# Optimization experiments

Hardware: AMD Instinct MI355X
Metric: run time of the kernel (lower is better)

Reference implementation:

```python
import jax, jax.numpy as jnp
import numpy as np
from jax import lax

ORDER = 6
SAMPLES = 64
TOPK = 512
STRIDE = 2          # contour features are stride-2 w.r.t. input ('1' level)
NMS_THRESH = 0.2
REF_ITERS = 4
REF_MARGIN = 3.0
HC = WC = 256       # contour-feature grid
HF = WF = 512       # full-res (refinement) grid


def conv2d(x, w, b=None, pad=0):
    # x: [B,C,H,W], w: [O,I,kh,kw]
    y = lax.conv_general_dilated(x, w, (1, 1), [(pad, pad), (pad, pad)],
                                 dimension_numbers=("NCHW", "OIHW", "NCHW"))
    if b is not None:
        y = y + b[None, :, None, None]
    return y


def setup_inputs() -> dict:
    key = jax.random.key(0)
    ks = jax.random.split(key, 16)
    s = 0.05
    d = {
        "contour_features": jax.random.normal(ks[0], (4, 64, HC, WC), jnp.float32),
        "enc_score_features": jax.random.normal(ks[1], (4, 64, HC, WC), jnp.float32),
        "refinement_features": jax.random.normal(ks[2], (4, 32, HF, WF), jnp.float32),
        "enc_refinement_features": jax.random.normal(ks[3], (4, 32, HF, WF), jnp.float32),
        # learned params
        "w_score_reduce": jax.random.normal(ks[4], (64, 128, 1, 1)) * s,
        "w_score": jax.random.normal(ks[5], (2, 64, 7, 7)) * s,
        "b_score": jnp.zeros((2,), jnp.float32),
        "w_loc": jax.random.normal(ks[6], (2, 64, 7, 7)) * s,
        "b_loc": jnp.zeros((2,), jnp.float32),
        "w_fourier": jax.random.normal(ks[7], (ORDER * 4, 64, 7, 7)) * s,
        "b_fourier": jnp.zeros((ORDER * 4,), jnp.float32),
        "w_ref_reduce": jax.random.normal(ks[8], (32, 64, 1, 1)) * s,
        "w_ref": jax.random.normal(ks[9], (2, 32, 7, 7)) * s,
        "b_ref": jnp.zeros((2,), jnp.float32),
    }
    return d


def _pairwise_iou(boxes):
    # boxes: [K,4] as (x1,y1,x2,y2)
    x1, y1, x2, y2 = boxes[:, 0], boxes[:, 1], boxes[:, 2], boxes[:, 3]
    area = jnp.maximum(x2 - x1, 0.) * jnp.maximum(y2 - y1, 0.)
    ix1 = jnp.maximum(x1[:, None], x1[None, :])
    iy1 = jnp.maximum(y1[:, None], y1[None, :])
    ix2 = jnp.minimum(x2[:, None], x2[None, :])
    iy2 = jnp.minimum(y2[:, None], y2[None, :])
    inter = jnp.maximum(ix2 - ix1, 0.) * jnp.maximum(iy2 - iy1, 0.)
    union = area[:, None] + area[None, :] - inter
    return inter / jnp.maximum(union, 1e-8)


def _nms_keep(boxes, valid):
    # boxes sorted by descending score. Sequential greedy NMS.
    iou = _pairwise_iou(boxes)  # [K,K]
    idx = jnp.arange(TOPK)

    def body(i, keep):
        sup = (iou[i] > NMS_THRESH) & keep[i] & (idx > i)
        return keep & ~sup

    keep = lax.fori_loop(0, TOPK, body, valid)
    return keep


def _forward(contour_features, enc_score_features, refinement_features,
             enc_refinement_features, w_score_reduce, w_score, b_score,
             w_loc, b_loc, w_fourier, b_fourier, w_ref_reduce, w_ref, b_ref):
    B = contour_features.shape[0]
    # ---- dense heads (CPNCore.forward) ----
    sf = conv2d(jnp.concatenate([contour_features, enc_score_features], 1), w_score_reduce)
    score_logits = conv2d(sf, w_score, b_score, pad=3)            # [B,2,HC,WC]
    log_scores = jax.nn.log_softmax(score_logits, axis=1)
    locations = conv2d(contour_features, w_loc, b_loc, pad=3)     # [B,2,HC,WC]
    fourier = conv2d(contour_features, w_fourier, b_fourier, pad=3)  # [B,4*ORDER,HC,WC]

    rf = conv2d(jnp.concatenate([refinement_features, enc_refinement_features], 1), w_ref_reduce)
    refinement = jnp.tanh(conv2d(rf, w_ref, b_ref, pad=3)) * REF_MARGIN  # [B,2,HF,WF]

    # ---- proposal selection: top-K foreground scores ----
    fg = jnp.exp(log_scores[:, 1])                                # [B,HC,WC]
    fg_flat = fg.reshape(B, -1)
    top_scores, top_idx = lax.top_k(fg_flat, TOPK)                # [B,K] sorted desc
    valid = top_scores > 0.5                                      # score_thresh

    gy = (top_idx // WC).astype(jnp.float32)
    gx = (top_idx % WC).astype(jnp.float32)

    def gather_ch(t):  # t: [B,C,HC,WC] -> [B,K,C]
        C = t.shape[1]
        tf = t.reshape(B, C, -1)
        out = jnp.take_along_axis(tf, top_idx[:, None, :].repeat(C, axis=1), axis=2)
        return out.transpose(0, 2, 1)

    loc = gather_ch(locations)                                    # [B,K,2] (x,y offsets)
    fr = gather_ch(fourier).reshape(B, TOPK, ORDER, 4)            # a_x,b_x,a_y,b_y

    cx = (gx + loc[..., 0]) * STRIDE
    cy = (gy + loc[..., 1]) * STRIDE

    # ---- fourier -> contour sampling ----
    t = jnp.arange(SAMPLES, dtype=jnp.float32) / SAMPLES
    k = jnp.arange(1, ORDER + 1, dtype=jnp.float32)
    ang = 2.0 * jnp.pi * k[:, None] * t[None, :]                  # [ORDER,SAMPLES]
    cos, sin = jnp.cos(ang), jnp.sin(ang)
    px = jnp.einsum('bko,os->bks', fr[..., 0], cos) + jnp.einsum('bko,os->bks', fr[..., 1], sin)
    py = jnp.einsum('bko,os->bks', fr[..., 2], cos) + jnp.einsum('bko,os->bks', fr[..., 3], sin)
    contour = jnp.stack([px * STRIDE + cx[..., None], py * STRIDE + cy[..., None]], -1)  # [B,K,S,2]

    # ---- iterative local refinement (nearest-neighbor gather) ----
    ref_flat = refinement.reshape(B, 2, -1)
    for _ in range(REF_ITERS):
        xi = jnp.clip(jnp.round(contour[..., 0]), 0, WF - 1).astype(jnp.int32)
        yi = jnp.clip(jnp.round(contour[..., 1]), 0, HF - 1).astype(jnp.int32)
        flat = (yi * WF + xi).reshape(B, 1, -1)                   # [B,1,K*S]
        off = jnp.take_along_axis(ref_flat, flat.repeat(2, axis=1), axis=2)
        off = off.reshape(B, 2, TOPK, SAMPLES).transpose(0, 2, 3, 1)  # [B,K,S,2]
        contour = contour + off

    # ---- boxes + NMS ----
    boxes = jnp.concatenate([contour.min(axis=2), contour.max(axis=2)], -1)  # [B,K,4]
    keep = jax.vmap(_nms_keep)(boxes, valid)
    return contour, top_scores, keep, boxes


def reference(contour_features, enc_score_features, refinement_features,
              enc_refinement_features, w_score_reduce, w_score, b_score,
              w_loc, b_loc, w_fourier, b_fourier, w_ref_reduce, w_ref, b_ref):
    return _forward(contour_features, enc_score_features, refinement_features,
                    enc_refinement_features, w_score_reduce, w_score, b_score,
                    w_loc, b_loc, w_fourier, b_fourier, w_ref_reduce, w_ref, b_ref)
```

## Files before the change

kernel.cpp:

```cpp
#include <hip/hip_runtime.h>
#include <math.h>

#define WS_D     0ull
#define WS_REF   1048576ull
#define WS_SPART 9437184ull
#define WS_WSE   13631488ull
#define WS_WRE   13731840ull
#define WS_WG    13782016ull
#define WS_TIDX  14108160ull
#define WS_GATH  14116352ull
#define WS_TRIG  14329344ull
#define WS_CLIST 14332416ull
#define WS_CNT   14365184ull
#define WS_PAIRS 14365200ull
#define WS_WRE32 14430736ull
#define WS_WSE32 14455824ull
#define WS_END   14506000ull

__global__ __launch_bounds__(256) void cpn_prep_kernel(
    const float* __restrict__ w_score_reduce, const float* __restrict__ w_score,
    const float* __restrict__ w_loc, const float* __restrict__ w_fourier,
    const float* __restrict__ w_ref_reduce, const float* __restrict__ w_ref,
    double* __restrict__ wse, double* __restrict__ wre, float* __restrict__ wg,
    float* __restrict__ trig, float* __restrict__ wre32, float* __restrict__ wse32)
{
    int i = blockIdx.x * 256 + threadIdx.x;
    if (i < 12544) {
        int o = i / 6272;
        int rem = i % 6272;
        int c = rem / 49, r = rem % 49;
        double a = 0.0;
        for (int m = 0; m < 64; ++m)
            a += (double)w_score[(o*64 + m)*49 + r] * (double)w_score_reduce[m*128 + c];
        wse[i] = a;
    } else if (i < 12544 + 6272) {
        int t = i - 12544;
        int o = t / 3136;
        int rem = t % 3136;
        int c = rem / 49, r = rem % 49;
        double a = 0.0;
        for (int m = 0; m < 32; ++m)
            a += (double)w_ref[(o*32 + m)*49 + r] * (double)w_ref_reduce[m*64 + c];
        wre[t] = a;
    } else if (i < 12544 + 6272 + 81536) {
        int t = i - 18816;
        int tap = t / 26, o = t % 26;
        wg[t] = (o < 2) ? w_loc[o*3136 + tap] : w_fourier[(o - 2)*3136 + tap];
    } else if (i < 100352 + 768) {
        int t = i - 100352;
        int cs = t / 384;
        int k = (t % 384) / 64, s = t % 64;
        const float TWO_PI_F = (float)6.283185307179586;
        float a1 = TWO_PI_F * (float)(k + 1);
        float tf = (float)s * 0.015625f;
        float ang = a1 * tf;
        double av = (double)ang;
        trig[t] = (cs == 0) ? (float)cos(av) : (float)sin(av);
    } else if (i < 101120 + 6272) {
        int t = i - 101120;
        int c = t / 98, r98 = t % 98;
        int ky = r98 / 14, q = r98 % 14;
        int kx = q >> 1, o = q & 1;
        int rr = ky*7 + kx;
        double a = 0.0;
        for (int m = 0; m < 32; ++m)
            a += (double)w_ref[(o*32 + m)*49 + rr] * (double)w_ref_reduce[m*64 + c];
        wre32[t] = (float)a;
    } else if (i < 107392 + 12544) {
        int t = i - 107392;
        int c = t / 98, r98 = t % 98;
        int ky = r98 / 14, q = r98 % 14;
        int kx = q >> 1, o = q & 1;
        int rr = ky*7 + kx;
        double a = 0.0;
        for (int m = 0; m < 64; ++m)
            a += (double)w_score[(o*64 + m)*49 + rr] * (double)w_score_reduce[m*128 + c];
        wse32[t] = (float)a;
    }
}

__global__ __launch_bounds__(512) void cpn_score_dense_kernel(
    const float* __restrict__ cf, const float* __restrict__ esf,
    const float* __restrict__ wse32, float2* __restrict__ partial)
{
    __shared__ __align__(16) float spatch[2][1672];
    const int tid  = threadIdx.x;
    const int t2   = tid & 255;
    const int h    = tid >> 8;
    const int b    = blockIdx.z >> 1;
    const int srch = blockIdx.z & 1;
    const float* src = srch ? esf : cf;
    const float* sbase = src + ((size_t)(b*64 + h*32) << 16);
    const int row0 = blockIdx.y * 32;
    const int col0 = blockIdx.x * 32;
    const int ty   = t2 >> 3;
    const int txg  = t2 & 7;
    const int cbase = srch*64 + h*32;

    float acc0[4] = {0.f,0.f,0.f,0.f};
    float acc1[4] = {0.f,0.f,0.f,0.f};
    float sreg[6];

    {
        #pragma unroll
        for (int k = 0; k < 6; ++k) {
            int i = k*256 + t2; float v = 0.f;
            if (i < 1520) {
                int r = i/40, j = i%40;
                int gy = row0 - 3 + r, gx = col0 - 4 + j;
                if ((unsigned)gy < 256u && (unsigned)gx < 256u) v = sbase[gy*256 + gx];
            }
            sreg[k] = v;
        }
    }

    for (int c = 0; c < 32; ++c) {
        #pragma unroll
        for (int k = 0; k < 6; ++k) {
            int i = k*256 + t2;
            if (i < 1520) spatch[h][(i/40)*44 + (i%40)] = sreg[k];
        }
        __syncthreads();
        if (c + 1 < 32) {
            const float* sp = sbase + ((size_t)(c+1) << 16);
            #pragma unroll
            for (int k = 0; k < 6; ++k) {
                int i = k*256 + t2; float v = 0.f;
                if (i < 1520) {
                    int r = i/40, j = i%40;
                    int gy = row0 - 3 + r, gx = col0 - 4 + j;
                    if ((unsigned)gy < 256u && (unsigned)gx < 256u) v = sp[gy*256 + gx];
                }
                sreg[k] = v;
            }
        }
        int cg = __builtin_amdgcn_readfirstlane(cbase + c);
        const float* wc = wse32 + cg*98;
        #pragma unroll
        for (int ky = 0; ky < 7; ++ky) {
            const float4* pr4 = reinterpret_cast<const float4*>(&spatch[h][(ty+ky)*44 + txg*4]);
            float4 A = pr4[0], B2 = pr4[1], C2 = pr4[2];
            float rv[12] = {A.x,A.y,A.z,A.w,B2.x,B2.y,B2.z,B2.w,C2.x,C2.y,C2.z,C2.w};
            const float* wp = wc + ky*14;
            float wv[14];
            #pragma unroll
            for (int q = 0; q < 14; ++q) wv[q] = wp[q];
            #pragma unroll
            for (int kx = 0; kx < 7; ++kx) {
                float w0 = wv[2*kx], w1 = wv[2*kx+1];
                #pragma unroll
                for (int p = 0; p < 4; ++p) {
                    float v = rv[p + kx + 1];
                    acc0[p] = fmaf(w0, v, acc0[p]);
                    acc1[p] = fmaf(w1, v, acc1[p]);
                }
            }
        }
        __syncthreads();
    }

    float* cmb = &spatch[0][0];
    if (h == 1) {
        #pragma unroll
        for (int p = 0; p < 4; ++p) { cmb[t2*8 + p] = acc0[p]; cmb[t2*8 + 4 + p] = acc1[p]; }
    }
    __syncthreads();
    if (h == 0) {
        int y = row0 + ty;
        #pragma unroll
        for (int p = 0; p < 4; ++p) {
            float s0 = acc0[p] + cmb[t2*8 + p];
            float s1 = acc1[p] + cmb[t2*8 + 4 + p];
            int x = col0 + txg*4 + p;
            float2 v; v.x = s0; v.y = s1;
            partial[(size_t)(srch*4 + b)*65536 + y*256 + x] = v;
        }
    }
}

__global__ __launch_bounds__(256) void cpn_dcomb_kernel(
    const float2* __restrict__ partial, float* __restrict__ d)
{
    int i = blockIdx.x * 256 + threadIdx.x;
    int b = i >> 16, px = i & 65535;
    float2 p0 = partial[(size_t)b*65536 + px];
    float2 p1 = partial[(size_t)(4 + b)*65536 + px];
    float l0 = p0.x + p1.x;
    float l1 = p0.y + p1.y;
    d[i] = l1 - l0;
}

__global__ __launch_bounds__(512) void cpn_ref_conv_kernel(
    const float* __restrict__ rff, const float* __restrict__ erf,
    const float* __restrict__ wre32, const float* __restrict__ b_ref,
    float* __restrict__ refmap)
{
    __shared__ __align__(16) float4 patches[2][38][19];
    const int tid = threadIdx.x;
    const int t2  = tid & 255;
    const int h   = tid >> 8;
    const int b   = blockIdx.z;
    const int row0 = blockIdx.y * 32;
    const int col0 = blockIdx.x * 64;
    const int tyg = t2 & 31;
    const int txg = t2 >> 5;
    const float* sbase = (h ? erf : rff) + ((size_t)(b*32) << 18);

    int   st_r[3], st_f[3];
    long  st_off[3];
    bool  st_ok[3];
    #pragma unroll
    for (int k = 0; k < 3; ++k) {
        int i = k*256 + t2;
        int r = i / 18, f = i % 18;
        int gy = row0 - 3 + r, gx = col0 - 4 + 4*f;
        st_r[k] = r; st_f[k] = f;
        st_ok[k] = (i < 684) && ((unsigned)gy < 512u) && ((unsigned)gx < 509u);
        st_off[k] = (long)gy * 512 + gx;
    }

    float4 s4[3];
    {
        #pragma unroll
        for (int k = 0; k < 3; ++k) {
            float4 v = {0.f,0.f,0.f,0.f};
            if (st_ok[k]) v = *reinterpret_cast<const float4*>(sbase + st_off[k]);
            s4[k] = v;
        }
    }

    float acc0[8] = {0,0,0,0,0,0,0,0};
    float acc1[8] = {0,0,0,0,0,0,0,0};

    for (int c = 0; c < 32; ++c) {
        #pragma unroll
        for (int k = 0; k < 3; ++k) {
            int i = k*256 + t2;
            if (i < 684) patches[h][st_r[k]][st_f[k]] = s4[k];
        }
        __syncthreads();
        if (c + 1 < 32) {
            const float* sp = sbase + ((size_t)(c+1) << 18);
            #pragma unroll
            for (int k = 0; k < 3; ++k) {
                float4 v = {0.f,0.f,0.f,0.f};
                if (st_ok[k]) v = *reinterpret_cast<const float4*>(sp + st_off[k]);
                s4[k] = v;
            }
        }
        int cg = __builtin_amdgcn_readfirstlane(h*32 + c);
        const float* wc = wre32 + cg*98;
        #pragma unroll
        for (int pr = 0; pr < 7; ++pr) {
            int row = tyg + pr;
            float4 A  = patches[h][row][2*txg + 0];
            float4 B2 = patches[h][row][2*txg + 1];
            float4 C2 = patches[h][row][2*txg + 2];
            float4 D2 = patches[h][row][2*txg + 3];
            float rv[16] = {A.x,A.y,A.z,A.w,B2.x,B2.y,B2.z,B2.w,
                            C2.x,C2.y,C2.z,C2.w,D2.x,D2.y,D2.z,D2.w};
            const float* wp = wc + pr*14;
            float wv[14];
            #pragma unroll
            for (int q = 0; q < 14; ++q) wv[q] = wp[q];
            #pragma unroll
            for (int kx = 0; kx < 7; ++kx) {
                float w0 = wv[2*kx], w1 = wv[2*kx+1];
                #pragma unroll
                for (int p = 0; p < 8; ++p) {
                    float v = rv[p + kx + 1];
                    acc0[p] = fmaf(w0, v, acc0[p]);
                    acc1[p] = fmaf(w1, v, acc1[p]);
                }
            }
        }
        __syncthreads();
    }

    float* cmb = reinterpret_cast<float*>(&patches[0][0][0]);
    if (h == 1) {
        #pragma unroll
        for (int p = 0; p < 8; ++p) { cmb[t2*16 + p] = acc0[p]; cmb[t2*16 + 8 + p] = acc1[p]; }
    }
    __syncthreads();
    if (h == 0) {
        float br0 = b_ref[0], br1 = b_ref[1];
        int y = row0 + tyg;
        int x0 = col0 + txg*8;
        #pragma unroll
        for (int p = 0; p < 8; ++p) {
            float s0 = acc0[p] + cmb[t2*16 + p];
            float s1 = acc1[p] + cmb[t2*16 + 8 + p];
            refmap[((size_t)(b*2 + 0)*512 + y)*512 + x0 + p] = tanhf(s0 + br0) * 3.0f;
            refmap[((size_t)(b*2 + 1)*512 + y)*512 + x0 + p] = tanhf(s1 + br1) * 3.0f;
        }
    }
}

__device__ __forceinline__ void cpn_find_bucket(
    unsigned int* hist, unsigned int* seg, int nb, int target, int tid,
    int* s_bsel, int* s_cnt)
{
    int nseg = nb / 32;
    for (int t = tid; t < nseg; t += 1024) {
        unsigned int s = 0;
        for (int q = 0; q < 32; ++q) s += hist[t*32 + q];
        seg[t] = s;
    }
    __syncthreads();
    if (tid == 0) {
        int cum = 0, sg = 0;
        for (int jj = nseg - 1; jj >= 0; --jj) {
            int c = (int)seg[jj];
            if (cum + c >= target) { sg = jj; break; }
            cum += c;
        }
        int bs = sg*32;
        for (int jj = sg*32 + 31; jj >= sg*32; --jj) {
            int c = (int)hist[jj];
            if (cum + c >= target) { bs = jj; break; }
            cum += c;
        }
        *s_bsel = bs; *s_cnt = cum;
    }
    __syncthreads();
}

__device__ __forceinline__ unsigned int cpn_fkey(float v) {
    unsigned int u = __float_as_uint(v);
    return (u & 0x80000000u) ? ~u : (u | 0x80000000u);
}

__global__ __launch_bounds__(1024) void cpn_select_kernel(
    const float* __restrict__ d, int* __restrict__ clist, int* __restrict__ cnt)
{
    const int b = blockIdx.x;
    const int tid = threadIdx.x;
    const float* f = d + (size_t)b * 65536;

    __shared__ unsigned int hist[2048];
    __shared__ unsigned int seg[64];
    __shared__ int s_b, s_c, s_n;

    const int bitsA[3]  = {11,11,10};
    const int shiftA[3] = {21,10,0};

    unsigned int prefix = 0;
    int target = 512;
    for (int pass = 0; pass < 3; ++pass) {
        int sh = shiftA[pass], nb = 1 << bitsA[pass];
        for (int i = tid; i < 2048; i += 1024) hist[i] = 0;
        __syncthreads();
        if (pass == 0) {
            for (int i = tid; i < 65536; i += 1024) {
                unsigned int k = cpn_fkey(f[i]);
                atomicAdd(&hist[k >> 21], 1u);
            }
        } else {
            int hs = sh + bitsA[pass];
            for (int i = tid; i < 65536; i += 1024) {
                unsigned int k = cpn_fkey(f[i]);
                if ((k >> hs) == prefix)
                    atomicAdd(&hist[(k >> sh) & (nb-1)], 1u);
            }
        }
        __syncthreads();
        cpn_find_bucket(hist, seg, nb, target, tid, &s_b, &s_c);
        prefix = (prefix << bitsA[pass]) | (unsigned)s_b;
        target -= s_c;
    }
    float T = (prefix & 0x80000000u) ? __uint_as_float(prefix & 0x7FFFFFFFu)
                                     : __uint_as_float(~prefix);
    float tval = T - 0.0625f;

    if (tid == 0) s_n = 0;
    __syncthreads();
    for (int i = tid; i < 65536; i += 1024) {
        if (f[i] >= tval) {
            int q = atomicAdd(&s_n, 1);
            if (q < 2048) clist[b*2048 + q] = i;
        }
    }
    __syncthreads();
    if (tid == 0) cnt[b] = (s_n > 2048) ? 2048 : s_n;
}

__global__ __launch_bounds__(256) void cpn_recompute_kernel(
    const float* __restrict__ cf, const float* __restrict__ esf,
    const double* __restrict__ wse, const float* __restrict__ b_score,
    const int* __restrict__ clist, const int* __restrict__ cnt,
    uint2* __restrict__ pairs)
{
    const int b = blockIdx.y, q = blockIdx.x, tid = threadIdx.x;
    const int n = cnt[b];
    if (q >= n) {
        if (tid == 0) { uint2 pd; pd.x = 0u; pd.y = 0x7FFFFFFFu; pairs[b*2048 + q] = pd; }
        return;
    }
    const int idx = clist[b*2048 + q];
    const int gy = idx >> 8, gx = idx & 255;

    double L0 = 0.0, L1 = 0.0;
    for (int t = tid; t < 6272; t += 256) {
        int c = t / 49, r = t % 49, ky = r / 7, kx = r % 7;
        int y = gy + ky - 3, x = gx + kx - 3;
        float v = 0.f;
        if ((unsigned)y < 256u && (unsigned)x < 256u) {
            const float* src = (c < 64) ? cf : esf;
            v = src[((size_t)(b*64 + (c & 63)) << 16) + y*256 + x];
        }
        double dv = (double)v;
        L0 = fma(dv, wse[c*49 + r], L0);
        L1 = fma(dv, wse[6272 + c*49 + r], L1);
    }
    #pragma unroll
    for (int off = 32; off; off >>= 1) {
        L0 += __shfl_down(L0, off, 64);
        L1 += __shfl_down(L1, off, 64);
    }
    __shared__ double red[4][2];
    int w = tid >> 6, lane = tid & 63;
    if (lane == 0) { red[w][0] = L0; red[w][1] = L1; }
    __syncthreads();
    if (tid == 0) {
        double S0 = red[0][0] + red[1][0] + red[2][0] + red[3][0];
        double S1 = red[0][1] + red[1][1] + red[2][1] + red[3][1];
        float l0f = (float)(S0 + (double)b_score[0]);
        float l1f = (float)(S1 + (double)b_score[1]);
        float m  = fmaxf(l0f, l1f);
        float e0 = (float)exp((double)(l0f - m));
        float e1 = (float)exp((double)(l1f - m));
        float s  = e0 + e1;
        float lg = (float)log((double)s);
        float ls1 = (l1f - m) - lg;
        float fgv = (float)exp((double)ls1);
        uint2 pr; pr.x = __float_as_uint(fgv); pr.y = (unsigned)idx;
        pairs[b*2048 + q] = pr;
    }
}

__global__ __launch_bounds__(1024) void cpn_sortk_kernel(
    const uint2* __restrict__ pairs, int* __restrict__ tidx,
    float* __restrict__ tscores)
{
    const int b = blockIdx.x;
    const int tid = threadIdx.x;
    __shared__ unsigned int key[2048];
    __shared__ int sidx[2048];

    for (int q = tid; q < 2048; q += 1024) {
        uint2 pr = pairs[b*2048 + q];
        key[q] = pr.x; sidx[q] = (int)pr.y;
    }
    __syncthreads();
    for (int kk = 2; kk <= 2048; kk <<= 1)
        for (int jj = kk >> 1; jj > 0; jj >>= 1) {
            for (int i = tid; i < 2048; i += 1024) {
                int ixj = i ^ jj;
                if (ixj > i) {
                    unsigned int ka = key[i], kc = key[ixj];
                    int ia = sidx[i], ic = sidx[ixj];
                    bool up = ((i & kk) == 0);
                    bool aBefore = (ka > kc) || (ka == kc && ia < ic);
                    if (up ? !aBefore : aBefore) {
                        key[i] = kc; key[ixj] = ka;
                        sidx[i] = ic; sidx[ixj] = ia;
                    }
                }
            }
            __syncthreads();
        }
    for (int q = tid; q < 512; q += 1024) {
        tscores[b*512 + q] = __uint_as_float(key[q]);
        tidx[b*512 + q] = sidx[q];
    }
}

__global__ __launch_bounds__(256) void cpn_gather_conv_kernel(
    const float* __restrict__ cf, const float* __restrict__ wg,
    const float* __restrict__ b_loc, const float* __restrict__ b_fourier,
    const int* __restrict__ tidx, float* __restrict__ gath)
{
    const int b = blockIdx.y, p = blockIdx.x, tid = threadIdx.x;
    const int idx = tidx[b*512 + p];
    const int gy = idx >> 8, gx = idx & 255;

    double part[26];
    #pragma unroll
    for (int o = 0; o < 26; ++o) part[o] = 0.0;

    for (int t = tid; t < 3136; t += 256) {
        int c = t / 49, rr = t % 49, ky = rr / 7, kx = rr % 7;
        int y = gy + ky - 3, x = gx + kx - 3;
        float v = 0.f;
        if ((unsigned)y < 256u && (unsigned)x < 256u)
            v = cf[((size_t)(b*64 + c)*256 + y)*256 + x];
        const float* wr = wg + t*26;
        double dv = (double)v;
        #pragma unroll
        for (int o = 0; o < 26; ++o) part[o] = fma(dv, (double)wr[o], part[o]);
    }
    #pragma unroll
    for (int o = 0; o < 26; ++o)
        for (int off = 32; off; off >>= 1) part[o] += __shfl_down(part[o], off, 64);

    __shared__ double red[4][26];
    int w = tid >> 6, lane = tid & 63;
    if (lane == 0) {
        #pragma unroll
        for (int o = 0; o < 26; ++o) red[w][o] = part[o];
    }
    __syncthreads();
    if (tid < 26) {
        double s = red[0][tid] + red[1][tid] + red[2][tid] + red[3][tid];
        s += (tid < 2) ? (double)b_loc[tid] : (double)b_fourier[tid - 2];
        gath[((size_t)b*512 + p)*26 + tid] = (float)s;
    }
}

__global__ __launch_bounds__(64) void cpn_contour_kernel(
    const float* __restrict__ gath, const int* __restrict__ tidx,
    const float* __restrict__ refmap, const float* __restrict__ trig,
    float* __restrict__ out_contour, float* __restrict__ out_boxes)
{
    const int bp = blockIdx.x;
    const int b = bp >> 9;
    const int s = threadIdx.x;
    const float* g = gath + (size_t)bp * 26;
    const int idx = tidx[bp];
    const int gy = idx >> 8, gx = idx & 255;

    float cx = ((float)gx + g[0]) * 2.0f;
    float cy = ((float)gy + g[1]) * 2.0f;

    float sxc = 0.f, sxs = 0.f, syc = 0.f, sys = 0.f;
    #pragma unroll
    for (int k = 0; k < 6; ++k) {
        float cs = trig[k*64 + s];
        float sn = trig[384 + k*64 + s];
        float t0 = g[2 + k*4 + 0] * cs; asm volatile("" : "+v"(t0)); sxc += t0;
        float t1 = g[2 + k*4 + 1] * sn; asm volatile("" : "+v"(t1)); sxs += t1;
        float t2 = g[2 + k*4 + 2] * cs; asm volatile("" : "+v"(t2)); syc += t2;
        float t3 = g[2 + k*4 + 3] * sn; asm volatile("" : "+v"(t3)); sys += t3;
    }
    float px = sxc + sxs;
    float py = syc + sys;
    float x = px * 2.0f; asm volatile("" : "+v"(x)); x += cx;
    float y = py * 2.0f; asm volatile("" : "+v"(y)); y += cy;

    const float* r0 = refmap + (size_t)b * 2 * 262144;
    const float* r1 = r0 + 262144;
    #pragma unroll
    for (int it = 0; it < 4; ++it) {
        float xr = rintf(x); xr = fminf(fmaxf(xr, 0.f), 511.f);
        float yr = rintf(y); yr = fminf(fmaxf(yr, 0.f), 511.f);
        int xi = (int)xr, yi = (int)yr;
        x += r0[yi*512 + xi];
        y += r1[yi*512 + xi];
    }

    out_contour[((size_t)bp*64 + s)*2 + 0] = x;
    out_contour[((size_t)bp*64 + s)*2 + 1] = y;

    float mnx = x, mxx = x, mny = y, mxy = y;
    #pragma unroll
    for (int off = 32; off; off >>= 1) {
        mnx = fminf(mnx, __shfl_xor(mnx, off, 64));
        mny = fminf(mny, __shfl_xor(mny, off, 64));
        mxx = fmaxf(mxx, __shfl_xor(mxx, off, 64));
        mxy = fmaxf(mxy, __shfl_xor(mxy, off, 64));
    }
    if (s == 0) {
        out_boxes[bp*4 + 0] = mnx;
        out_boxes[bp*4 + 1] = mny;
        out_boxes[bp*4 + 2] = mxx;
        out_boxes[bp*4 + 3] = mxy;
    }
}

__global__ __launch_bounds__(512) void cpn_nms_kernel(
    const float* __restrict__ boxes, const float* __restrict__ scores,
    float* __restrict__ keep_out)
{
    const int b = blockIdx.x;
    const int j = threadIdx.x;
    __shared__ float X1[512], Y1[512], X2[512], Y2[512], AR[512];
    __shared__ int keep[512];

    const float* bb = boxes + b*512*4;
    float x1 = bb[j*4+0], y1 = bb[j*4+1], x2 = bb[j*4+2], y2 = bb[j*4+3];
    float aj = fmaxf(x2 - x1, 0.f) * fmaxf(y2 - y1, 0.f);
    X1[j] = x1; Y1[j] = y1; X2[j] = x2; Y2[j] = y2; AR[j] = aj;
    keep[j] = (scores[b*512 + j] > 0.5f) ? 1 : 0;
    __syncthreads();

    for (int i = 0; i < 512; ++i) {
        if (keep[i] && j > i) {
            float ix1 = fmaxf(x1, X1[i]);
            float iy1 = fmaxf(y1, Y1[i]);
            float ix2 = fminf(x2, X2[i]);
            float iy2 = fminf(y2, Y2[i]);
            float inter = fmaxf(ix2 - ix1, 0.f) * fmaxf(iy2 - iy1, 0.f);
            float uni = (aj + AR[i]) - inter;
            float iou = inter / fmaxf(uni, 1e-8f);
            if (iou > 0.2f) keep[j] = 0;
        }
        __syncthreads();
    }
    keep_out[b*512 + j] = keep[j] ? 1.0f : 0.0f;
}

extern "C" void kernel_launch(void* const* d_in, const int* in_sizes, int n_in,
                              void* d_out, int out_size, void* d_ws, size_t ws_size,
                              hipStream_t stream)
{
    if (ws_size < WS_END) return;

    const float* cf   = (const float*)d_in[0];
    const float* esf  = (const float*)d_in[1];
    const float* rff  = (const float*)d_in[2];
    const float* erf  = (const float*)d_in[3];
    const float* w_sr = (const float*)d_in[4];
    const float* w_s  = (const float*)d_in[5];
    const float* b_s  = (const float*)d_in[6];
    const float* w_l  = (const float*)d_in[7];
    const float* b_l  = (const float*)d_in[8];
    const float* w_f  = (const float*)d_in[9];
    const float* b_f  = (const float*)d_in[10];
    const float* w_rr = (const float*)d_in[11];
    const float* w_r  = (const float*)d_in[12];
    const float* b_r  = (const float*)d_in[13];

    char* ws = (char*)d_ws;
    float*  dbuf = (float*)(ws + WS_D);
    float*  refm = (float*)(ws + WS_REF);
    float2* spart = (float2*)(ws + WS_SPART);
    double* wse  = (double*)(ws + WS_WSE);
    double* wre  = (double*)(ws + WS_WRE);
    float*  wg   = (float*)(ws + WS_WG);
    int*    tidx = (int*)(ws + WS_TIDX);
    float*  gath = (float*)(ws + WS_GATH);
    float*  trig = (float*)(ws + WS_TRIG);
    int*    clist = (int*)(ws + WS_CLIST);
    int*    cnt  = (int*)(ws + WS_CNT);
    uint2*  pairs = (uint2*)(ws + WS_PAIRS);
    float*  wre32 = (float*)(ws + WS_WRE32);
    float*  wse32 = (float*)(ws + WS_WSE32);

    float* out_contour = (float*)d_out;
    float* out_scores  = out_contour + 262144;
    float* out_keep    = out_scores + 2048;
    float* out_boxes   = out_keep + 2048;

    cpn_prep_kernel<<<dim3(469), dim3(256), 0, stream>>>(
        w_sr, w_s, w_l, w_f, w_rr, w_r, wse, wre, wg, trig, wre32, wse32);
    cpn_score_dense_kernel<<<dim3(8, 8, 8), dim3(512), 0, stream>>>(
        cf, esf, wse32, spart);
    cpn_ref_conv_kernel<<<dim3(8, 16, 4), dim3(512), 0, stream>>>(
        rff, erf, wre32, b_r, refm);
    cpn_dcomb_kernel<<<dim3(1024), dim3(256), 0, stream>>>(spart, dbuf);
    cpn_select_kernel<<<dim3(4), dim3(1024), 0, stream>>>(dbuf, clist, cnt);
    cpn_recompute_kernel<<<dim3(2048, 4), dim3(256), 0, stream>>>(
        cf, esf, wse, b_s, clist, cnt, pairs);
    cpn_sortk_kernel<<<dim3(4), dim3(1024), 0, stream>>>(pairs, tidx, out_scores);
    cpn_gather_conv_kernel<<<dim3(512, 4), dim3(256), 0, stream>>>(
        cf, wg, b_l, b_f, tidx, gath);
    cpn_contour_kernel<<<dim3(2048), dim3(64), 0, stream>>>(
        gath, tidx, refm, trig, out_contour, out_boxes);
    cpn_nms_kernel<<<dim3(4), dim3(512), 0, stream>>>(
        out_boxes, out_scores, out_keep);
}
```

Measured before the change: 673.4 us.

## Stage conv input patches via direct global-to-LDS loads with double buffering

Both the dense score conv and the refinement conv now load input channel patches with global_load_lds straight into a double-buffered shared-memory patch, replacing the register staging and separate LDS store. This removes VGPR staging and the store step, and drops one barrier per channel iteration, so the next channel's load overlaps compute on the current buffer. Out-of-bounds slots are zeroed once at start and never rewritten. The score-conv patch also switches to float4 rows with 40-wide stride and 4-aligned loads. A risk is correctness of the async LDS writes, since there is no explicit vmcnt wait before the single barrier that precedes use.

```diff
diff --git a/kernel.cpp b/kernel.cpp
--- a/kernel.cpp
+++ b/kernel.cpp
@@ -16,6 +16,9 @@
 #define WS_WRE32 14430736ull
 #define WS_WSE32 14455824ull
 #define WS_END   14506000ull
+
+typedef __attribute__((address_space(1))) const void cpn_gv;
+typedef __attribute__((address_space(3))) void cpn_lv;
 
 __global__ __launch_bounds__(256) void cpn_prep_kernel(
     const float* __restrict__ w_score_reduce, const float* __restrict__ w_score,
@@ -83,10 +86,11 @@
     const float* __restrict__ cf, const float* __restrict__ esf,
     const float* __restrict__ wse32, float2* __restrict__ partial)
 {
-    __shared__ __align__(16) float spatch[2][1672];
+    __shared__ __align__(16) float4 patch[2][2][380];
     const int tid  = threadIdx.x;
     const int t2   = tid & 255;
     const int h    = tid >> 8;
+    const int wv   = t2 >> 6;
     const int b    = blockIdx.z >> 1;
     const int srch = blockIdx.z & 1;
     const float* src = srch ? esf : cf;
@@ -97,57 +101,59 @@
     const int txg  = t2 & 7;
     const int cbase = srch*64 + h*32;
 
+    long st_off[2];
+    bool st_ok[2];
+    #pragma unroll
+    for (int k = 0; k < 2; ++k) {
+        int i = k*256 + t2;
+        int r = i / 10, f = i % 10;
+        int gy = row0 - 3 + r, gx = col0 - 4 + 4*f;
+        st_ok[k] = (i < 380) && ((unsigned)gy < 256u) && ((unsigned)gx < 253u);
+        st_off[k] = (long)gy * 256 + gx;
+    }
+
+    float4 z4 = {0.f,0.f,0.f,0.f};
+    for (int i = tid; i < 2*2*380; i += 512) (&patch[0][0][0])[i] = z4;
+    __syncthreads();
+
+    #pragma unroll
+    for (int k = 0; k < 2; ++k)
+        if (st_ok[k])
+            __builtin_amdgcn_global_load_lds(
+                (cpn_gv*)(sbase + st_off[k]),
+                (cpn_lv*)&patch[h][0][k*256 + wv*64], 16, 0, 0);
+
     float acc0[4] = {0.f,0.f,0.f,0.f};
     float acc1[4] = {0.f,0.f,0.f,0.f};
-    float sreg[6];
-
-    {
-        #pragma unroll
-        for (int k = 0; k < 6; ++k) {
-            int i = k*256 + t2; float v = 0.f;
-            if (i < 1520) {
-                int r = i/40, j = i%40;
-                int gy = row0 - 3 + r, gx = col0 - 4 + j;
-                if ((unsigned)gy < 256u && (unsigned)gx < 256u) v = sbase[gy*256 + gx];
-            }
-            sreg[k] = v;
-        }
-    }
 
     for (int c = 0; c < 32; ++c) {
-        #pragma unroll
-        for (int k = 0; k < 6; ++k) {
-            int i = k*256 + t2;
-            if (i < 1520) spatch[h][(i/40)*44 + (i%40)] = sreg[k];
-        }
         __syncthreads();
         if (c + 1 < 32) {
             const float* sp = sbase + ((size_t)(c+1) << 16);
             #pragma unroll
-            for (int k = 0; k < 6; ++k) {
-                int i = k*256 + t2; float v = 0.f;
-                if (i < 1520) {
-                    int r = i/40, j = i%40;
-                    int gy = row0 - 3 + r, gx = col0 - 4 + j;
-                    if ((unsigned)gy < 256u && (unsigned)gx < 256u) v = sp[gy*256 + gx];
-                }
-                sreg[k] = v;
-            }
+            for (int k = 0; k < 2; ++k)
+                if (st_ok[k])
+                    __builtin_amdgcn_global_load_lds(
+                        (cpn_gv*)(sp + st_off[k]),
+                        (cpn_lv*)&patch[h][(c+1)&1][k*256 + wv*64], 16, 0, 0);
         }
         int cg = __builtin_amdgcn_readfirstlane(cbase + c);
         const float* wc = wse32 + cg*98;
+        const float4* pb = &patch[h][c & 1][0];
         #pragma unroll
         for (int ky = 0; ky < 7; ++ky) {
-            const float4* pr4 = reinterpret_cast<const float4*>(&spatch[h][(ty+ky)*44 + txg*4]);
-            float4 A = pr4[0], B2 = pr4[1], C2 = pr4[2];
+            int row = ty + ky;
+            float4 A  = pb[row*10 + txg + 0];
+            float4 B2 = pb[row*10 + txg + 1];
+            float4 C2 = pb[row*10 + txg + 2];
             float rv[12] = {A.x,A.y,A.z,A.w,B2.x,B2.y,B2.z,B2.w,C2.x,C2.y,C2.z,C2.w};
             const float* wp = wc + ky*14;
-            float wv[14];
+            float wv14[14];
             #pragma unroll
-            for (int q = 0; q < 14; ++q) wv[q] = wp[q];
+            for (int q = 0; q < 14; ++q) wv14[q] = wp[q];
             #pragma unroll
             for (int kx = 0; kx < 7; ++kx) {
-                float w0 = wv[2*kx], w1 = wv[2*kx+1];
+                float w0 = wv14[2*kx], w1 = wv14[2*kx+1];
                 #pragma unroll
                 for (int p = 0; p < 4; ++p) {
                     float v = rv[p + kx + 1];
@@ -156,10 +162,10 @@
                 }
             }
         }
-        __syncthreads();
-    }
-
-    float* cmb = &spatch[0][0];
+    }
+    __syncthreads();
+
+    float* cmb = reinterpret_cast<float*>(&patch[0][0][0]);
     if (h == 1) {
         #pragma unroll
         for (int p = 0; p < 4; ++p) { cmb[t2*8 + p] = acc0[p]; cmb[t2*8 + 4 + p] = acc1[p]; }
@@ -195,10 +201,11 @@
     const float* __restrict__ wre32, const float* __restrict__ b_ref,
     float* __restrict__ refmap)
 {
-    __shared__ __align__(16) float4 patches[2][38][19];
+    __shared__ __align__(16) float4 patch[2][2][684];
     const int tid = threadIdx.x;
     const int t2  = tid & 255;
     const int h   = tid >> 8;
+    const int wv  = t2 >> 6;
     const int b   = blockIdx.z;
     const int row0 = blockIdx.y * 32;
     const int col0 = blockIdx.x * 64;
@@ -206,66 +213,61 @@
     const int txg = t2 >> 5;
     const float* sbase = (h ? erf : rff) + ((size_t)(b*32) << 18);
 
-    int   st_r[3], st_f[3];
-    long  st_off[3];
-    bool  st_ok[3];
+    long st_off[3];
+    bool st_ok[3];
     #pragma unroll
     for (int k = 0; k < 3; ++k) {
         int i = k*256 + t2;
         int r = i / 18, f = i % 18;
         int gy = row0 - 3 + r, gx = col0 - 4 + 4*f;
-        st_r[k] = r; st_f[k] = f;
         st_ok[k] = (i < 684) && ((unsigned)gy < 512u) && ((unsigned)gx < 509u);
         st_off[k] = (long)gy * 512 + gx;
     }
 
-    float4 s4[3];
-    {
-        #pragma unroll
-        for (int k = 0; k < 3; ++k) {
-            float4 v = {0.f,0.f,0.f,0.f};
-            if (st_ok[k]) v = *reinterpret_cast<const float4*>(sbase + st_off[k]);
-            s4[k] = v;
-        }
-    }
+    float4 z4 = {0.f,0.f,0.f,0.f};
+    for (int i = tid; i < 2*2*684; i += 512) (&patch[0][0][0])[i] = z4;
+    __syncthreads();
+
+    #pragma unroll
+    for (int k = 0; k < 3; ++k)
+        if (st_ok[k])
+            __builtin_amdgcn_global_load_lds(
+                (cpn_gv*)(sbase + st_off[k]),
+                (cpn_lv*)&patch[h][0][k*256 + wv*64], 16, 0, 0);
 
     float acc0[8] = {0,0,0,0,0,0,0,0};
     float acc1[8] = {0,0,0,0,0,0,0,0};
 
     for (int c = 0; c < 32; ++c) {
-        #pragma unroll
-        for (int k = 0; k < 3; ++k) {
-            int i = k*256 + t2;
-            if (i < 684) patches[h][st_r[k]][st_f[k]] = s4[k];
-        }
         __syncthreads();
         if (c + 1 < 32) {
             const float* sp = sbase + ((size_t)(c+1) << 18);
             #pragma unroll
-            for (int k = 0; k < 3; ++k) {
-                float4 v = {0.f,0.f,0.f,0.f};
-                if (st_ok[k]) v = *reinterpret_cast<const float4*>(sp + st_off[k]);
-                s4[k] = v;
-            }
+            for (int k = 0; k < 3; ++k)
+                if (st_ok[k])
+                    __builtin_amdgcn_global_load_lds(
+                        (cpn_gv*)(sp + st_off[k]),
+                        (cpn_lv*)&patch[h][(c+1)&1][k*256 + wv*64], 16, 0, 0);
         }
         int cg = __builtin_amdgcn_readfirstlane(h*32 + c);
         const float* wc = wre32 + cg*98;
+        const float4* pb = &patch[h][c & 1][0];
         #pragma unroll
         for (int pr = 0; pr < 7; ++pr) {
             int row = tyg + pr;
-            float4 A  = patches[h][row][2*txg + 0];
-            float4 B2 = patches[h][row][2*txg + 1];
-            float4 C2 = patches[h][row][2*txg + 2];
-            float4 D2 = patches[h][row][2*txg + 3];
+            float4 A  = pb[row*18 + 2*txg + 0];
+            float4 B2 = pb[row*18 + 2*txg + 1];
+            float4 C2 = pb[row*18 + 2*txg + 2];
+            float4 D2 = pb[row*18 + 2*txg + 3];
             float rv[16] = {A.x,A.y,A.z,A.w,B2.x,B2.y,B2.z,B2.w,
                             C2.x,C2.y,C2.z,C2.w,D2.x,D2.y,D2.z,D2.w};
             const float* wp = wc + pr*14;
-            float wv[14];
+            float wv14[14];
             #pragma unroll
-            for (int q = 0; q < 14; ++q) wv[q] = wp[q];
+            for (int q = 0; q < 14; ++q) wv14[q] = wp[q];
             #pragma unroll
             for (int kx = 0; kx < 7; ++kx) {
-                float w0 = wv[2*kx], w1 = wv[2*kx+1];
+                float w0 = wv14[2*kx], w1 = wv14[2*kx+1];
                 #pragma unroll
                 for (int p = 0; p < 8; ++p) {
                     float v = rv[p + kx + 1];
@@ -274,10 +276,10 @@
                 }
             }
         }
-        __syncthreads();
-    }
-
-    float* cmb = reinterpret_cast<float*>(&patches[0][0][0]);
+    }
+    __syncthreads();
+
+    float* cmb = reinterpret_cast<float*>(&patch[0][0][0]);
     if (h == 1) {
         #pragma unroll
         for (int p = 0; p < 8; ++p) { cmb[t2*16 + p] = acc0[p]; cmb[t2*16 + 8 + p] = acc1[p]; }
```

Result: slower. 823.4 us (+22.3%).
